# Optimization experiments

Measured on AMD Instinct MI355X. Metric: run time of the kernel, lower is better.

The kernel has to match this reference:

```python
import jax, jax.numpy as jnp
import numpy as np
from jax import lax

K = 3          # local attention window (kernel_size)
DIL = 1        # dilation
PAD = DIL * (K - 1) // 2  # 'same' padding for the window gather


def _patches(t):
    # t: [B, C, H, W] -> [B, C, K*K, H, W] local neighborhoods (zero-padded)
    B, C, H, W = t.shape
    p = lax.conv_general_dilated_patches(
        t, filter_shape=(K, K), window_strides=(1, 1),
        padding=((PAD, PAD), (PAD, PAD)), rhs_dilation=(DIL, DIL))
    # output channels ordered (C, K, K) -> [B, C, K*K, H, W]
    return p.reshape(B, C, K * K, H, W)


def setup_inputs() -> dict:
    key = jax.random.key(0)
    k1, k2, k3, k4 = jax.random.split(key, 4)
    B, C, H, W = 4, 64, 256, 256
    x = jax.random.normal(k1, (B, C, H, W), dtype=jnp.float32)
    w_qkv = jax.random.normal(k2, (3 * C, C), dtype=jnp.float32) * 0.1
    b_qkv = jax.random.normal(k3, (3 * C,), dtype=jnp.float32) * 0.1
    w_mlp = jax.random.normal(k4, (C, C, K, K), dtype=jnp.float32) * 0.1
    return {"x": x, "w_qkv": w_qkv, "b_qkv": b_qkv, "w_mlp": w_mlp}


def reference(x, w_qkv, b_qkv, w_mlp):
    C = x.shape[1]
    scale = C ** (-0.5)
    # 1x1 qkv conv
    qkv = jnp.einsum('bchw,oc->bohw', x, w_qkv) + b_qkv[None, :, None, None]
    q, k, v = jnp.split(qkv, 3, axis=1)
    # conv1: local window QK^T -> [B, K*K, H, W]
    kp = _patches(k)                                   # [B,C,K*K,H,W]
    dots = jnp.einsum('bchw,bcnhw->bnhw', q, kp) * scale
    attn = jax.nn.softmax(dots, axis=1)                # softmax over window dim
    # conv2: attention-weighted aggregation of v neighbors -> [B,C,H,W]
    vp = _patches(v)
    out = jnp.einsum('bnhw,bcnhw->bchw', attn, vp)
    out = out + x                                      # residual
    # mlp: 3x3 conv, stride 1, padding 1, no bias
    out = lax.conv_general_dilated(out, w_mlp, (1, 1), ((PAD, PAD), (PAD, PAD)))
    return jax.nn.relu(out)
```

## Files before the change

### kernel.cpp

```cpp
#include <hip/hip_runtime.h>
#include <hip/hip_bf16.h>

typedef __attribute__((ext_vector_type(8))) short short8;
typedef __attribute__((ext_vector_type(4))) short short4_;
typedef __attribute__((ext_vector_type(4))) float float4_;
typedef __attribute__((ext_vector_type(4))) unsigned int uint4_;

#define CH 64
#define HH 256
#define WW 256
#define HW (HH*WW)
#define CHW (CH*HW)

#define TW 16
#define TH 8
#define XPW 20
#define XPH 12
#define NXP 240
#define OPW 18
#define OPH 10
#define NOP 180

#define XLS 72
#define KQ2 40
#define VS  32
#define O1S 64
#define TSF 33

#define QB2_OFF 9600
#define O1_OFF  7680
#define SMEM_SHORTS 19200

#define WSQ_SHORTS 12288
#define WSM_SHORTS 36864

__device__ __forceinline__ float blo(unsigned u) {
    return __uint_as_float(u << 16);
}
__device__ __forceinline__ float bhi(unsigned u) {
    return __uint_as_float(u & 0xffff0000u);
}
__device__ __forceinline__ short f2bs(float f) {
    __hip_bfloat16 h = __float2bfloat16(f);
    short s; __builtin_memcpy(&s, &h, 2); return s;
}
__device__ __forceinline__ unsigned pack2(float a, float b) {
    return (unsigned)(unsigned short)f2bs(a) |
           ((unsigned)(unsigned short)f2bs(b) << 16);
}

__device__ __forceinline__ int xls_idx(int pix, int c) {
    int g = ((c >> 3) ^ ((pix >> 2) & 7));
    return pix * XLS + g * 8 + (c & 7);
}
__device__ __forceinline__ int o1_idx(int pix, int c) {
    int g = (((c >> 3) ^ pix) & 7);
    return pix * O1S + g * 8 + (c & 7);
}
__device__ __forceinline__ int vswz(int p) {
    return (p ^ (p >> 2)) & 3;
}

#if defined(__has_builtin)
#if __has_builtin(__builtin_amdgcn_fdot2_f32_bf16)
#define HAS_BF16_DOT2 1
#endif
#endif
#ifdef HAS_BF16_DOT2
typedef __bf16 bf16x2 __attribute__((ext_vector_type(2)));
__device__ __forceinline__ float dot2acc(unsigned a, unsigned b, float acc) {
    return __builtin_amdgcn_fdot2_f32_bf16(__builtin_bit_cast(bf16x2, a),
                                           __builtin_bit_cast(bf16x2, b),
                                           acc, false);
}
#else
__device__ __forceinline__ float dot2acc(unsigned a, unsigned b, float acc) {
    acc += blo(a) * blo(b);
    acc += bhi(a) * bhi(b);
    return acc;
}
#endif

__global__ void prep_pack(const float* __restrict__ wqkv,
                          const float* __restrict__ wmlp,
                          short* __restrict__ wsq, short* __restrict__ wsm) {
    int idx = blockIdx.x * blockDim.x + threadIdx.x;
    int stride = gridDim.x * blockDim.x;
    for (int e = idx; e < WSQ_SHORTS; e += stride) {
        int j = e & 7, lane = (e >> 3) & 63;
        int ks = (e >> 9) & 1, q16 = (e >> 10) & 3, sec = e >> 12;
        int row = sec*64 + q16*16 + (lane & 15);
        int kk  = ks*32 + (lane >> 4)*8 + j;
        wsq[e] = f2bs(wqkv[(size_t)row*64 + kk]);
    }
    for (int e = idx; e < WSM_SHORTS; e += stride) {
        int j = e & 7, lane = (e >> 3) & 63;
        int rest = e >> 9;
        int nt = rest / 18, ks = rest % 18;
        int o   = nt*16 + (lane & 15);
        int cin = (ks & 1)*32 + (lane >> 4)*8 + j;
        int tap = ks >> 1;
        wsm[e] = f2bs(wmlp[(size_t)o*576 + cin*9 + tap]);
    }
}

__global__ __launch_bounds__(256, 3) void fused_mfma(
    const float* __restrict__ x, const short* __restrict__ wsq,
    const float* __restrict__ bqkv, const short* __restrict__ wsm,
    float* __restrict__ out)
{
    __shared__ __align__(16) short smem[SMEM_SHORTS];
    short* xls   = smem;
    short* kbuf2 = smem;
    short* qbuf2 = smem + QB2_OFF;
    short* vbuf  = smem;
    short* o1b   = smem + O1_OFF;
    float* tbA   = (float*)smem;
    float* tbB   = (float*)smem + 4224;

    const int t    = threadIdx.x;
    const int w    = t >> 6;
    const int lane = t & 63;
    const int n16  = lane & 15;
    const int quad = lane >> 4;

    const int d   = blockIdx.x + (blockIdx.y << 4) + (blockIdx.z << 9);
    const int nn  = ((d & 7) << 8) | (d >> 3);
    const int b   = nn >> 9;
    const int rem = nn & 511;
    const int gy0 = (rem >> 4) * TH;
    const int gx0 = (rem & 15) * TW;
    const float* xb = x + (size_t)b * CHW;

    for (int slot = t; slot < 32*12*6; slot += 256) {
        int s6 = slot % 6, y = (slot / 6) % 12, c2 = slot / 72;
        int c  = c2 * 2;
        int gy = gy0 - 2 + y;
        int gxb = gx0 - 4 + s6*4;
        float v0[4], v1[4];
        bool gyok = (unsigned)gy < HH;
        if (gyok && gxb >= 0 && gxb + 3 < WW) {
            float4_ f0 = *(const float4_*)(xb + (size_t)c*HW + gy*WW + gxb);
            float4_ f1 = *(const float4_*)(xb + (size_t)(c+1)*HW + gy*WW + gxb);
            #pragma unroll
            for (int i = 0; i < 4; ++i) { v0[i] = f0[i]; v1[i] = f1[i]; }
        } else {
            #pragma unroll
            for (int i = 0; i < 4; ++i) {
                int gx = gxb + i;
                bool ok = gyok && (unsigned)gx < WW;
                v0[i] = ok ? xb[(size_t)c*HW + gy*WW + gx] : 0.f;
                v1[i] = ok ? xb[(size_t)(c+1)*HW + gy*WW + gx] : 0.f;
            }
        }
        #pragma unroll
        for (int i = 0; i < 4; ++i) {
            int pxc = s6*4 + i - 2;
            if ((unsigned)pxc < XPW)
                *(unsigned*)&xls[xls_idx(y*XPW + pxc, c)] = pack2(v0[i], v1[i]);
        }
    }
    __syncthreads();

    unsigned okb = 0;
    #pragma unroll
    for (int i = 0; i < 4; ++i) {
        int p = (w*4 + i)*16 + n16;
        if (p < NXP) {
            int gy = gy0 - 2 + p / XPW, gx = gx0 - 2 + p % XPW;
            if (((unsigned)gy < HH) && ((unsigned)gx < WW))
                okb |= 1u << i;
        }
    }

    short8 afr[4][2];
    #pragma unroll
    for (int i = 0; i < 4; ++i) {
        int p = (w*4 + i)*16 + n16;
        int pr = (p < NXP) ? p : 0;
        #pragma unroll
        for (int ks = 0; ks < 2; ++ks)
            afr[i][ks] = *(const short8*)&xls[xls_idx(pr, ks*32 + quad*8)];
    }
    const int op_py = t / OPW, op_px = t % OPW;
    const int ogy = gy0 - 1 + op_py, ogx = gx0 - 1 + op_px;
    const bool oin = (t < NOP) && ((unsigned)ogy < HH) && ((unsigned)ogx < WW);
    const int xpix = (op_py + 1)*XPW + (op_px + 1);
    short8 resi[8];
    if (t < NOP) {
        #pragma unroll
        for (int g = 0; g < 8; ++g)
            resi[g] = *(const short8*)&xls[xls_idx(xpix, g*8)];
    }
    __syncthreads();

    auto wload = [&](int sec, int q16, int ks) -> short8 {
        return *(const short8*)&wsq[(((sec*4 + q16)*2 + ks) << 9) + lane*8];
    };
    auto bload = [&](int base) -> float4_ {
        return *(const float4_*)&bqkv[base + quad*4];
    };
    auto gemm_k = [&](short8 w0, short8 w1, float4_ b4, int coff) {
        #pragma unroll
        for (int i = 0; i < 4; ++i) {
            int p = (w*4 + i)*16 + n16;
            float4_ c = {0.f, 0.f, 0.f, 0.f};
            c = __builtin_amdgcn_mfma_f32_16x16x32_bf16(w0, afr[i][0], c, 0, 0, 0);
            c = __builtin_amdgcn_mfma_f32_16x16x32_bf16(w1, afr[i][1], c, 0, 0, 0);
            if (p < NXP) {
                bool ok = (okb >> i) & 1u;
                short4_ s;
                #pragma unroll
                for (int r = 0; r < 4; ++r) s[r] = ok ? f2bs(c[r] + b4[r]) : (short)0;
                *(short4_*)&kbuf2[p*KQ2 + coff + quad*4] = s;
            }
        }
    };
    auto gemm_v = [&](short8 w0, short8 w1, float4_ b4, int coff) {
        #pragma unroll
        for (int i = 0; i < 4; ++i) {
            int p = (w*4 + i)*16 + n16;
            float4_ c = {0.f, 0.f, 0.f, 0.f};
            c = __builtin_amdgcn_mfma_f32_16x16x32_bf16(w0, afr[i][0], c, 0, 0, 0);
            c = __builtin_amdgcn_mfma_f32_16x16x32_bf16(w1, afr[i][1], c, 0, 0, 0);
            if (p < NXP) {
                bool ok = (okb >> i) & 1u;
                short4_ s;
                #pragma unroll
                for (int r = 0; r < 4; ++r) s[r] = ok ? f2bs(c[r] + b4[r]) : (short)0;
                int cc = coff + quad*4;
                int idx = p*VS + ((((cc >> 3) ^ vswz(p)) & 3) << 3) + (cc & 7);
                *(short4_*)&vbuf[idx] = s;
            }
        }
    };
    auto gemm_q = [&](short8 w0, short8 w1, float4_ b4, int coff) {
        #pragma unroll
        for (int i = 0; i < 4; ++i) {
            int p = (w*4 + i)*16 + n16;
            float4_ c = {0.f, 0.f, 0.f, 0.f};
            c = __builtin_amdgcn_mfma_f32_16x16x32_bf16(w0, afr[i][0], c, 0, 0, 0);
            c = __builtin_amdgcn_mfma_f32_16x16x32_bf16(w1, afr[i][1], c, 0, 0, 0);
            int py = p / XPW, px = p % XPW;
            if ((unsigned)(py - 1) < (unsigned)OPH &&
                (unsigned)(px - 1) < (unsigned)OPW) {
                int op = (py - 1)*OPW + (px - 1);
                short4_ s;
                #pragma unroll
                for (int r = 0; r < 4; ++r) s[r] = f2bs(c[r] + b4[r]);
                *(short4_*)&qbuf2[op*KQ2 + coff + quad*4] = s;
            }
        }
    };

    float dots[9];
    #pragma unroll
    for (int n2 = 0; n2 < 9; ++n2) dots[n2] = 0.f;

    short8 pw0 = wload(0,0,0), pw1 = wload(0,0,1);

    #pragma unroll
    for (int rr = 0; rr < 2; ++rr) {
        {
            short8 b0 = wload(0, 2*rr+1, 0), b1 = wload(0, 2*rr+1, 1);
            gemm_q(pw0, pw1, bload((2*rr)*16), 0);
            gemm_q(b0,  b1,  bload((2*rr+1)*16), 16);
            short8 c0 = wload(1, 2*rr,   0), c1 = wload(1, 2*rr,   1);
            short8 d0 = wload(1, 2*rr+1, 0), d1 = wload(1, 2*rr+1, 1);
            gemm_k(c0, c1, bload(64 + (2*rr)*16),  0);
            gemm_k(d0, d1, bload(64 + (2*rr+1)*16), 16);
        }
        __syncthreads();
        if (rr == 0) { pw0 = wload(0, 2, 0); pw1 = wload(0, 2, 1); }
        else         { pw0 = wload(2, 0, 0); pw1 = wload(2, 0, 1); }
        if (oin) {
            uint4_ qa = *(const uint4_*)&qbuf2[t*KQ2];
            uint4_ qb = *(const uint4_*)&qbuf2[t*KQ2 + 8];
            uint4_ qc = *(const uint4_*)&qbuf2[t*KQ2 + 16];
            uint4_ qd = *(const uint4_*)&qbuf2[t*KQ2 + 24];
            #pragma unroll
            for (int n2 = 0; n2 < 9; ++n2) {
                int np = xpix + (n2/3 - 1)*XPW + (n2%3 - 1);
                uint4_ ka = *(const uint4_*)&kbuf2[np*KQ2];
                uint4_ kb = *(const uint4_*)&kbuf2[np*KQ2 + 8];
                uint4_ kc = *(const uint4_*)&kbuf2[np*KQ2 + 16];
                uint4_ kd = *(const uint4_*)&kbuf2[np*KQ2 + 24];
                float sA = dots[n2], sB = 0.f, sC = 0.f, sD = 0.f;
                #pragma unroll
                for (int j = 0; j < 4; ++j) sA = dot2acc(qa[j], ka[j], sA);
                #pragma unroll
                for (int j = 0; j < 4; ++j) sB = dot2acc(qb[j], kb[j], sB);
                #pragma unroll
                for (int j = 0; j < 4; ++j) sC = dot2acc(qc[j], kc[j], sC);
                #pragma unroll
                for (int j = 0; j < 4; ++j) sD = dot2acc(qd[j], kd[j], sD);
                dots[n2] = (sA + sB) + (sC + sD);
            }
        }
        __syncthreads();
    }

    float attn[9];
    if (oin) {
        float mx = -1e30f;
        #pragma unroll
        for (int n2 = 0; n2 < 9; ++n2) { dots[n2] *= 0.125f; mx = fmaxf(mx, dots[n2]); }
        float se = 0.f;
        #pragma unroll
        for (int n2 = 0; n2 < 9; ++n2) { attn[n2] = __expf(dots[n2] - mx); se += attn[n2]; }
        float inv = 1.f / se;
        #pragma unroll
        for (int n2 = 0; n2 < 9; ++n2) attn[n2] *= inv;
    }

    #pragma unroll
    for (int rr2 = 0; rr2 < 2; ++rr2) {
        {
            short8 b2 = wload(2, 2*rr2+1, 0), b3 = wload(2, 2*rr2+1, 1);
            gemm_v(pw0, pw1, bload(128 + (2*rr2)*16), 0);
            gemm_v(b2,  b3,  bload(128 + (2*rr2+1)*16), 16);
        }
        __syncthreads();
        if (rr2 == 0) { pw0 = wload(2, 2, 0); pw1 = wload(2, 2, 1); }
        if (t < NOP) {
            #pragma unroll
            for (int h2 = 0; h2 < 2; ++h2) {
                const int kg = rr2*2 + h2;
                short8 s0, s1;
                if (oin) {
                    float o1[16];
                    uint4_ r0 = __builtin_bit_cast(uint4_, resi[kg*2]);
                    uint4_ r1 = __builtin_bit_cast(uint4_, resi[kg*2 + 1]);
                    #pragma unroll
                    for (int j = 0; j < 4; ++j) {
                        o1[2*j]     = blo(r0[j]); o1[2*j + 1]     = bhi(r0[j]);
                        o1[8 + 2*j] = blo(r1[j]); o1[8 + 2*j + 1] = bhi(r1[j]);
                    }
                    #pragma unroll
                    for (int n2 = 0; n2 < 9; ++n2) {
                        float a = attn[n2];
                        int np = xpix + (n2/3 - 1)*XPW + (n2%3 - 1);
                        int sw = vswz(np);
                        uint4_ va = *(const uint4_*)&vbuf[np*VS + (((h2*2)   ^ sw) << 3)];
                        uint4_ vb = *(const uint4_*)&vbuf[np*VS + (((h2*2+1) ^ sw) << 3)];
                        #pragma unroll
                        for (int j = 0; j < 4; ++j) {
                            o1[2*j]         += a * blo(va[j]);
                            o1[2*j + 1]     += a * bhi(va[j]);
                            o1[8 + 2*j]     += a * blo(vb[j]);
                            o1[8 + 2*j + 1] += a * bhi(vb[j]);
                        }
                    }
                    #pragma unroll
                    for (int j = 0; j < 8; ++j) {
                        s0[j] = f2bs(o1[j]);
                        s1[j] = f2bs(o1[8 + j]);
                    }
                } else {
                    #pragma unroll
                    for (int j = 0; j < 8; ++j) { s0[j] = 0; s1[j] = 0; }
                }
                *(short8*)&o1b[o1_idx(t, kg*16)]     = s0;
                *(short8*)&o1b[o1_idx(t, kg*16 + 8)] = s1;
            }
        }
        __syncthreads();
    }

    float4_ acc[4][2];
    #pragma unroll
    for (int nt = 0; nt < 4; ++nt) {
        acc[nt][0] = (float4_){0.f,0.f,0.f,0.f};
        acc[nt][1] = (float4_){0.f,0.f,0.f,0.f};
    }
    const int mtc0 = w*2, mtc1 = w*2 + 1;
    for (int ks = 0; ks < 18; ++ks) {
        int tap = ks >> 1;
        int dy = tap/3 - 1, dx = tap%3 - 1;
        int cin0 = (ks & 1)*32 + quad*8;
        int pixA = (mtc0 + 1 + dy)*OPW + (n16 + 1 + dx);
        int pixB = (mtc1 + 1 + dy)*OPW + (n16 + 1 + dx);
        short8 a0 = *(const short8*)&o1b[o1_idx(pixA, cin0)];
        short8 a1 = *(const short8*)&o1b[o1_idx(pixB, cin0)];
        #pragma unroll
        for (int nt = 0; nt < 4; ++nt) {
            short8 bb = *(const short8*)&wsm[((nt*18 + ks) << 9) + lane*8];
            acc[nt][0] = __builtin_amdgcn_mfma_f32_16x16x32_bf16(a0, bb, acc[nt][0], 0, 0, 0);
            acc[nt][1] = __builtin_amdgcn_mfma_f32_16x16x32_bf16(a1, bb, acc[nt][1], 0, 0, 0);
        }
    }
    __syncthreads();

    #pragma unroll
    for (int ntl = 0; ntl < 2; ++ntl)
        #pragma unroll
        for (int r = 0; r < 4; ++r) {
            tbA[(mtc0*16 + quad*4 + r)*TSF + ntl*16 + n16] = fmaxf(acc[ntl][0][r], 0.f);
            tbA[(mtc1*16 + quad*4 + r)*TSF + ntl*16 + n16] = fmaxf(acc[ntl][1][r], 0.f);
        }
    __syncthreads();
    {
        int pl = t & 127, oh = t >> 7;
        int ty_ = pl >> 4, tx_ = pl & 15;
        float* op = out + (size_t)b*CHW + (size_t)(oh*16)*HW
                    + (size_t)(gy0 + ty_)*WW + (gx0 + tx_);
        #pragma unroll
        for (int ii = 0; ii < 16; ++ii)
            op[(size_t)ii*HW] = tbA[pl*TSF + oh*16 + ii];
    }
    #pragma unroll
    for (int ntl = 0; ntl < 2; ++ntl)
        #pragma unroll
        for (int r = 0; r < 4; ++r) {
            tbB[(mtc0*16 + quad*4 + r)*TSF + ntl*16 + n16] = fmaxf(acc[2+ntl][0][r], 0.f);
            tbB[(mtc1*16 + quad*4 + r)*TSF + ntl*16 + n16] = fmaxf(acc[2+ntl][1][r], 0.f);
        }
    __syncthreads();
    {
        int pl = t & 127, oh = t >> 7;
        int ty_ = pl >> 4, tx_ = pl & 15;
        float* op = out + (size_t)b*CHW + (size_t)(32 + oh*16)*HW
                    + (size_t)(gy0 + ty_)*WW + (gx0 + tx_);
        #pragma unroll
        for (int ii = 0; ii < 16; ++ii)
            op[(size_t)ii*HW] = tbB[pl*TSF + oh*16 + ii];
    }
}

extern "C" void kernel_launch(void* const* d_in, const int* in_sizes, int n_in,
                              void* d_out, int out_size, void* d_ws, size_t ws_size,
                              hipStream_t stream) {
    const float* x    = (const float*)d_in[0];
    const float* wqkv = (const float*)d_in[1];
    const float* bqkv = (const float*)d_in[2];
    const float* wmlp = (const float*)d_in[3];
    float* outp = (float*)d_out;

    short* wsq = (short*)d_ws;
    short* wsm = wsq + WSQ_SHORTS;

    prep_pack<<<128, 256, 0, stream>>>(wqkv, wmlp, wsq, wsm);

    dim3 grid(WW/TW, HH/TH, 4);
    fused_mfma<<<grid, 256, 0, stream>>>(x, wsq, bqkv, wsm, outp);
}
```

Before: 235.6 us.

## Keep Q in registers, compute dots on halo pixels, vectorize output stores

Q projections stay in MFMA output registers instead of being written to LDS. Partial QK dot products are computed per halo pixel over each lane's channel slice and reduced across lanes with shuffles. K is double-buffered in two LDS regions so one sync per round is dropped, and the V/PV rounds are restructured to match. The epilogue writes a channel-major tile and stores float4 vectors to global memory instead of scalar strided stores. In exchange it adds cross-lane shuffles, clamped neighbor indices, and a larger live register set for qp.

```diff
diff --git a/kernel.cpp b/kernel.cpp
--- a/kernel.cpp
+++ b/kernel.cpp
@@ -4,6 +4,7 @@
 typedef __attribute__((ext_vector_type(8))) short short8;
 typedef __attribute__((ext_vector_type(4))) short short4_;
 typedef __attribute__((ext_vector_type(4))) float float4_;
+typedef __attribute__((ext_vector_type(2))) unsigned int uint2_;
 typedef __attribute__((ext_vector_type(4))) unsigned int uint4_;
 
 #define CH 64
@@ -25,9 +26,9 @@
 #define KQ2 40
 #define VS  32
 #define O1S 64
-#define TSF 33
-
-#define QB2_OFF 9600
+#define TBS 132
+
+#define KB_OFF  9600
 #define O1_OFF  7680
 #define SMEM_SHORTS 19200
 
@@ -110,13 +111,12 @@
     float* __restrict__ out)
 {
     __shared__ __align__(16) short smem[SMEM_SHORTS];
-    short* xls   = smem;
-    short* kbuf2 = smem;
-    short* qbuf2 = smem + QB2_OFF;
-    short* vbuf  = smem;
-    short* o1b   = smem + O1_OFF;
-    float* tbA   = (float*)smem;
-    float* tbB   = (float*)smem + 4224;
+    short* xls  = smem;
+    short* kA   = smem;
+    short* kB   = smem + KB_OFF;
+    short* vbuf = smem;
+    short* o1b  = smem + O1_OFF;
+    float* tb2  = (float*)smem;
 
     const int t    = threadIdx.x;
     const int w    = t >> 6;
@@ -182,29 +182,44 @@
         for (int ks = 0; ks < 2; ++ks)
             afr[i][ks] = *(const short8*)&xls[xls_idx(pr, ks*32 + quad*8)];
     }
-    const int op_py = t / OPW, op_px = t % OPW;
-    const int ogy = gy0 - 1 + op_py, ogx = gx0 - 1 + op_px;
-    const bool oin = (t < NOP) && ((unsigned)ogy < HH) && ((unsigned)ogx < WW);
-    const int xpix = (op_py + 1)*XPW + (op_px + 1);
+    const int hpy = t / XPW, hpx = t % XPW;
+    const bool inter = (t < NXP) &&
+                       ((unsigned)(hpy - 1) < (unsigned)OPH) &&
+                       ((unsigned)(hpx - 1) < (unsigned)OPW);
+    const int ogy = gy0 - 2 + hpy, ogx = gx0 - 2 + hpx;
+    const bool oin = inter && ((unsigned)ogy < HH) && ((unsigned)ogx < WW);
+    const int opix = (hpy - 1)*OPW + (hpx - 1);
     short8 resi[8];
-    if (t < NOP) {
+    if (inter) {
         #pragma unroll
         for (int g = 0; g < 8; ++g)
-            resi[g] = *(const short8*)&xls[xls_idx(xpix, g*8)];
+            resi[g] = *(const short8*)&xls[xls_idx(t, g*8)];
     }
     __syncthreads();
 
     auto wload = [&](int sec, int q16, int ks) -> short8 {
         return *(const short8*)&wsq[(((sec*4 + q16)*2 + ks) << 9) + lane*8];
     };
-    auto bload = [&](int base) -> float4_ {
+    auto bload4 = [&](int base) -> float4_ {
         return *(const float4_*)&bqkv[base + quad*4];
     };
-    auto gemm_k = [&](short8 w0, short8 w1, float4_ b4, int coff) {
+
+    unsigned qp[4][4];
+    auto gemm_qreg = [&](short8 w0, short8 w1, float4_ b4, int half) {
+        #pragma unroll
+        for (int i = 0; i < 4; ++i) {
+            float4_ c = {0.f,0.f,0.f,0.f};
+            c = __builtin_amdgcn_mfma_f32_16x16x32_bf16(w0, afr[i][0], c, 0, 0, 0);
+            c = __builtin_amdgcn_mfma_f32_16x16x32_bf16(w1, afr[i][1], c, 0, 0, 0);
+            qp[i][half*2 + 0] = pack2(c[0] + b4[0], c[1] + b4[1]);
+            qp[i][half*2 + 1] = pack2(c[2] + b4[2], c[3] + b4[3]);
+        }
+    };
+    auto gemm_kbuf = [&](short8 w0, short8 w1, float4_ b4, short* dst, int coff) {
         #pragma unroll
         for (int i = 0; i < 4; ++i) {
             int p = (w*4 + i)*16 + n16;
-            float4_ c = {0.f, 0.f, 0.f, 0.f};
+            float4_ c = {0.f,0.f,0.f,0.f};
             c = __builtin_amdgcn_mfma_f32_16x16x32_bf16(w0, afr[i][0], c, 0, 0, 0);
             c = __builtin_amdgcn_mfma_f32_16x16x32_bf16(w1, afr[i][1], c, 0, 0, 0);
             if (p < NXP) {
@@ -212,15 +227,15 @@
                 short4_ s;
                 #pragma unroll
                 for (int r = 0; r < 4; ++r) s[r] = ok ? f2bs(c[r] + b4[r]) : (short)0;
-                *(short4_*)&kbuf2[p*KQ2 + coff + quad*4] = s;
-            }
-        }
-    };
-    auto gemm_v = [&](short8 w0, short8 w1, float4_ b4, int coff) {
+                *(short4_*)&dst[p*KQ2 + coff + quad*4] = s;
+            }
+        }
+    };
+    auto gemm_vbuf = [&](short8 w0, short8 w1, float4_ b4, int coff) {
         #pragma unroll
         for (int i = 0; i < 4; ++i) {
             int p = (w*4 + i)*16 + n16;
-            float4_ c = {0.f, 0.f, 0.f, 0.f};
+            float4_ c = {0.f,0.f,0.f,0.f};
             c = __builtin_amdgcn_mfma_f32_16x16x32_bf16(w0, afr[i][0], c, 0, 0, 0);
             c = __builtin_amdgcn_mfma_f32_16x16x32_bf16(w1, afr[i][1], c, 0, 0, 0);
             if (p < NXP) {
@@ -234,71 +249,81 @@
             }
         }
     };
-    auto gemm_q = [&](short8 w0, short8 w1, float4_ b4, int coff) {
-        #pragma unroll
-        for (int i = 0; i < 4; ++i) {
-            int p = (w*4 + i)*16 + n16;
-            float4_ c = {0.f, 0.f, 0.f, 0.f};
-            c = __builtin_amdgcn_mfma_f32_16x16x32_bf16(w0, afr[i][0], c, 0, 0, 0);
-            c = __builtin_amdgcn_mfma_f32_16x16x32_bf16(w1, afr[i][1], c, 0, 0, 0);
-            int py = p / XPW, px = p % XPW;
-            if ((unsigned)(py - 1) < (unsigned)OPH &&
-                (unsigned)(px - 1) < (unsigned)OPW) {
-                int op = (py - 1)*OPW + (px - 1);
-                short4_ s;
+
+    float dots[9];
+    #pragma unroll
+    for (int n2 = 0; n2 < 9; ++n2) dots[n2] = 0.f;
+
+    const bool hi2 = (quad & 2) != 0, hi1 = (quad & 1) != 0;
+    auto dot_partial = [&](const short* kb) {
+        #pragma unroll
+        for (int dy = 0; dy < 3; ++dy) {
+            float P[4][3];
+            #pragma unroll
+            for (int i = 0; i < 4; ++i) {
+                int pi = (w*4 + i)*16 + n16;
                 #pragma unroll
-                for (int r = 0; r < 4; ++r) s[r] = f2bs(c[r] + b4[r]);
-                *(short4_*)&qbuf2[op*KQ2 + coff + quad*4] = s;
-            }
-        }
-    };
-
-    float dots[9];
-    #pragma unroll
-    for (int n2 = 0; n2 < 9; ++n2) dots[n2] = 0.f;
-
-    short8 pw0 = wload(0,0,0), pw1 = wload(0,0,1);
-
-    #pragma unroll
-    for (int rr = 0; rr < 2; ++rr) {
-        {
-            short8 b0 = wload(0, 2*rr+1, 0), b1 = wload(0, 2*rr+1, 1);
-            gemm_q(pw0, pw1, bload((2*rr)*16), 0);
-            gemm_q(b0,  b1,  bload((2*rr+1)*16), 16);
-            short8 c0 = wload(1, 2*rr,   0), c1 = wload(1, 2*rr,   1);
-            short8 d0 = wload(1, 2*rr+1, 0), d1 = wload(1, 2*rr+1, 1);
-            gemm_k(c0, c1, bload(64 + (2*rr)*16),  0);
-            gemm_k(d0, d1, bload(64 + (2*rr+1)*16), 16);
-        }
-        __syncthreads();
-        if (rr == 0) { pw0 = wload(0, 2, 0); pw1 = wload(0, 2, 1); }
-        else         { pw0 = wload(2, 0, 0); pw1 = wload(2, 0, 1); }
-        if (oin) {
-            uint4_ qa = *(const uint4_*)&qbuf2[t*KQ2];
-            uint4_ qb = *(const uint4_*)&qbuf2[t*KQ2 + 8];
-            uint4_ qc = *(const uint4_*)&qbuf2[t*KQ2 + 16];
-            uint4_ qd = *(const uint4_*)&qbuf2[t*KQ2 + 24];
-            #pragma unroll
-            for (int n2 = 0; n2 < 9; ++n2) {
-                int np = xpix + (n2/3 - 1)*XPW + (n2%3 - 1);
-                uint4_ ka = *(const uint4_*)&kbuf2[np*KQ2];
-                uint4_ kb = *(const uint4_*)&kbuf2[np*KQ2 + 8];
-                uint4_ kc = *(const uint4_*)&kbuf2[np*KQ2 + 16];
-                uint4_ kd = *(const uint4_*)&kbuf2[np*KQ2 + 24];
-                float sA = dots[n2], sB = 0.f, sC = 0.f, sD = 0.f;
-                #pragma unroll
-                for (int j = 0; j < 4; ++j) sA = dot2acc(qa[j], ka[j], sA);
-                #pragma unroll
-                for (int j = 0; j < 4; ++j) sB = dot2acc(qb[j], kb[j], sB);
-                #pragma unroll
-                for (int j = 0; j < 4; ++j) sC = dot2acc(qc[j], kc[j], sC);
-                #pragma unroll
-                for (int j = 0; j < 4; ++j) sD = dot2acc(qd[j], kd[j], sD);
-                dots[n2] = (sA + sB) + (sC + sD);
-            }
-        }
-        __syncthreads();
-    }
+                for (int dx = 0; dx < 3; ++dx) {
+                    int np = pi + (dy - 1)*XPW + (dx - 1);
+                    np = np < 0 ? 0 : (np > NXP-1 ? NXP-1 : np);
+                    uint2_ k0 = *(const uint2_*)&kb[np*KQ2 + quad*4];
+                    uint2_ k1 = *(const uint2_*)&kb[np*KQ2 + 16 + quad*4];
+                    float s = 0.f;
+                    s = dot2acc(qp[i][0], k0[0], s);
+                    s = dot2acc(qp[i][1], k0[1], s);
+                    s = dot2acc(qp[i][2], k1[0], s);
+                    s = dot2acc(qp[i][3], k1[1], s);
+                    P[i][dx] = s;
+                }
+            }
+            #pragma unroll
+            for (int dx = 0; dx < 3; ++dx) {
+                float own0 = hi2 ? P[2][dx] : P[0][dx];
+                float own1 = hi2 ? P[3][dx] : P[1][dx];
+                float snd0 = hi2 ? P[0][dx] : P[2][dx];
+                float snd1 = hi2 ? P[1][dx] : P[3][dx];
+                float S0 = own0 + __shfl_xor(snd0, 32);
+                float S1 = own1 + __shfl_xor(snd1, 32);
+                float own2 = hi1 ? S1 : S0;
+                float snd2 = hi1 ? S0 : S1;
+                dots[dy*3 + dx] += own2 + __shfl_xor(snd2, 16);
+            }
+        }
+    };
+
+    {
+        short8 a0 = wload(0,0,0), a1 = wload(0,0,1);
+        short8 a2 = wload(0,1,0), a3 = wload(0,1,1);
+        short8 k0 = wload(1,0,0), k1 = wload(1,0,1);
+        short8 k2 = wload(1,1,0), k3 = wload(1,1,1);
+        gemm_qreg(a0, a1, bload4(0), 0);
+        gemm_qreg(a2, a3, bload4(16), 1);
+        gemm_kbuf(k0, k1, bload4(64), kA, 0);
+        gemm_kbuf(k2, k3, bload4(64+16), kA, 16);
+    }
+    __syncthreads();
+
+    dot_partial(kA);
+    {
+        short8 a0 = wload(0,2,0), a1 = wload(0,2,1);
+        short8 a2 = wload(0,3,0), a3 = wload(0,3,1);
+        short8 k0 = wload(1,2,0), k1 = wload(1,2,1);
+        short8 k2 = wload(1,3,0), k3 = wload(1,3,1);
+        gemm_qreg(a0, a1, bload4(32), 0);
+        gemm_qreg(a2, a3, bload4(48), 1);
+        gemm_kbuf(k0, k1, bload4(64+32), kB, 0);
+        gemm_kbuf(k2, k3, bload4(64+48), kB, 16);
+    }
+    __syncthreads();
+
+    dot_partial(kB);
+    {
+        short8 v0 = wload(2,0,0), v1 = wload(2,0,1);
+        short8 v2 = wload(2,1,0), v3 = wload(2,1,1);
+        gemm_vbuf(v0, v1, bload4(128), 0);
+        gemm_vbuf(v2, v3, bload4(128+16), 16);
+    }
+    __syncthreads();
 
     float attn[9];
     if (oin) {
@@ -313,16 +338,8 @@
         for (int n2 = 0; n2 < 9; ++n2) attn[n2] *= inv;
     }
 
-    #pragma unroll
-    for (int rr2 = 0; rr2 < 2; ++rr2) {
-        {
-            short8 b2 = wload(2, 2*rr2+1, 0), b3 = wload(2, 2*rr2+1, 1);
-            gemm_v(pw0, pw1, bload(128 + (2*rr2)*16), 0);
-            gemm_v(b2,  b3,  bload(128 + (2*rr2+1)*16), 16);
-        }
-        __syncthreads();
-        if (rr2 == 0) { pw0 = wload(2, 2, 0); pw1 = wload(2, 2, 1); }
-        if (t < NOP) {
+    auto pv_round = [&](int rr2) {
+        if (inter) {
             #pragma unroll
             for (int h2 = 0; h2 < 2; ++h2) {
                 const int kg = rr2*2 + h2;
@@ -339,7 +356,7 @@
                     #pragma unroll
                     for (int n2 = 0; n2 < 9; ++n2) {
                         float a = attn[n2];
-                        int np = xpix + (n2/3 - 1)*XPW + (n2%3 - 1);
+                        int np = t + (n2/3 - 1)*XPW + (n2%3 - 1);
                         int sw = vswz(np);
                         uint4_ va = *(const uint4_*)&vbuf[np*VS + (((h2*2)   ^ sw) << 3)];
                         uint4_ vb = *(const uint4_*)&vbuf[np*VS + (((h2*2+1) ^ sw) << 3)];
@@ -360,12 +377,25 @@
                     #pragma unroll
                     for (int j = 0; j < 8; ++j) { s0[j] = 0; s1[j] = 0; }
                 }
-                *(short8*)&o1b[o1_idx(t, kg*16)]     = s0;
-                *(short8*)&o1b[o1_idx(t, kg*16 + 8)] = s1;
-            }
-        }
-        __syncthreads();
-    }
+                *(short8*)&o1b[o1_idx(opix, kg*16)]     = s0;
+                *(short8*)&o1b[o1_idx(opix, kg*16 + 8)] = s1;
+            }
+        }
+    };
+
+    pv_round(0);
+    __syncthreads();
+
+    {
+        short8 v0 = wload(2,2,0), v1 = wload(2,2,1);
+        short8 v2 = wload(2,3,0), v3 = wload(2,3,1);
+        gemm_vbuf(v0, v1, bload4(128+32), 0);
+        gemm_vbuf(v2, v3, bload4(128+48), 16);
+    }
+    __syncthreads();
+
+    pv_round(1);
+    __syncthreads();
 
     float4_ acc[4][2];
     #pragma unroll
@@ -392,38 +422,23 @@
     __syncthreads();
 
     #pragma unroll
-    for (int ntl = 0; ntl < 2; ++ntl)
-        #pragma unroll
-        for (int r = 0; r < 4; ++r) {
-            tbA[(mtc0*16 + quad*4 + r)*TSF + ntl*16 + n16] = fmaxf(acc[ntl][0][r], 0.f);
-            tbA[(mtc1*16 + quad*4 + r)*TSF + ntl*16 + n16] = fmaxf(acc[ntl][1][r], 0.f);
-        }
-    __syncthreads();
-    {
-        int pl = t & 127, oh = t >> 7;
-        int ty_ = pl >> 4, tx_ = pl & 15;
-        float* op = out + (size_t)b*CHW + (size_t)(oh*16)*HW
-                    + (size_t)(gy0 + ty_)*WW + (gx0 + tx_);
-        #pragma unroll
-        for (int ii = 0; ii < 16; ++ii)
-            op[(size_t)ii*HW] = tbA[pl*TSF + oh*16 + ii];
-    }
-    #pragma unroll
-    for (int ntl = 0; ntl < 2; ++ntl)
-        #pragma unroll
-        for (int r = 0; r < 4; ++r) {
-            tbB[(mtc0*16 + quad*4 + r)*TSF + ntl*16 + n16] = fmaxf(acc[2+ntl][0][r], 0.f);
-            tbB[(mtc1*16 + quad*4 + r)*TSF + ntl*16 + n16] = fmaxf(acc[2+ntl][1][r], 0.f);
-        }
-    __syncthreads();
-    {
-        int pl = t & 127, oh = t >> 7;
-        int ty_ = pl >> 4, tx_ = pl & 15;
-        float* op = out + (size_t)b*CHW + (size_t)(32 + oh*16)*HW
-                    + (size_t)(gy0 + ty_)*WW + (gx0 + tx_);
-        #pragma unroll
-        for (int ii = 0; ii < 16; ++ii)
-            op[(size_t)ii*HW] = tbB[pl*TSF + oh*16 + ii];
+    for (int nt = 0; nt < 4; ++nt)
+        #pragma unroll
+        for (int h = 0; h < 2; ++h) {
+            int mtc = w*2 + h;
+            float4_ rv;
+            #pragma unroll
+            for (int r = 0; r < 4; ++r) rv[r] = fmaxf(acc[nt][h][r], 0.f);
+            *(float4_*)&tb2[(nt*16 + n16)*TBS + mtc*16 + quad*4] = rv;
+        }
+    __syncthreads();
+    #pragma unroll
+    for (int k = 0; k < 8; ++k) {
+        int unit = t + k*256;
+        int ch = unit >> 5, y = (unit >> 2) & 7, xg = unit & 3;
+        float4_ v = *(const float4_*)&tb2[ch*TBS + y*16 + xg*4];
+        *(float4_*)(out + (size_t)b*CHW + (size_t)ch*HW
+                    + (size_t)(gy0 + y)*WW + (gx0 + xg*4)) = v;
     }
 }
 
```

Measured after the change: 251.8 us. +6.9%, slower.
